# Kernel tuning notes

Hardware: AMD Instinct MI355X
Metric: run time of the kernel (lower is better)

The kernel has to match this reference:

```python
import jax, jax.numpy as jnp
import numpy as np

B, S, D = 8, 4096, 1024
F = 4 * D  # expert hidden dim (internal_dim = d_model * 4)
E = 8      # num experts


def setup_inputs() -> dict:
    key = jax.random.key(0)
    ks = jax.random.split(key, 7)
    x = jax.random.normal(ks[0], (B, S, D), dtype=jnp.float32)
    expert_weights = jax.random.uniform(ks[1], (B, 1), dtype=jnp.float32)
    expert_indices = jax.random.randint(ks[2], (B, 1), 0, E)
    # Per-expert MLP params: Linear(D,F) -> GELU -> Linear(F,D)
    W1 = jax.random.normal(ks[3], (E, D, F), dtype=jnp.float32) / np.sqrt(D)
    b1 = jnp.zeros((E, F), dtype=jnp.float32)
    W2 = jax.random.normal(ks[4], (E, F, D), dtype=jnp.float32) / np.sqrt(F)
    b2 = jnp.zeros((E, D), dtype=jnp.float32)
    return {"x": x, "expert_weights": expert_weights, "W1": W1, "b1": b1,
            "W2": W2, "b2": b2, "expert_indices": expert_indices}


def reference(x, expert_weights, W1, b1, W2, b2, expert_indices):
    # Top-1 routing per sequence (router built with top_k=1):
    # each batch element b is processed by expert idx[b], output scaled by w[b].
    idx = expert_indices[:, 0]          # [B]
    w = expert_weights[:, 0]            # [B]
    w1 = W1[idx]                        # [B, D, F] gather of expert params
    w2 = W2[idx]                        # [B, F, D]
    h = jnp.einsum('bsd,bdf->bsf', x, w1) + b1[idx][:, None, :]
    h = jax.nn.gelu(h, approximate=False)  # torch nn.GELU default = exact erf
    y = jnp.einsum('bsf,bfd->bsd', h, w2) + b2[idx][:, None, :]
    # weighted scatter-combine: final_output[mask] += expert_output * w
    return y * w[:, None, None]
```

## Files before the change

kernel.cpp:

```cpp
#include <hip/hip_runtime.h>
#include <hip/hip_bf16.h>


#define B_ 8
#define S_ 4096
#define D_ 1024
#define F_ 4096
#define E_ 8

typedef __bf16 bf16x8 __attribute__((ext_vector_type(8)));
typedef float f32x4 __attribute__((ext_vector_type(4)));

__device__ __forceinline__ unsigned short f2bf(float f) {
  unsigned u = __float_as_uint(f);
  u += 0x7FFFu + ((u >> 16) & 1u);
  return (unsigned short)(u >> 16);
}

#define GLD16(g, l) __builtin_amdgcn_global_load_lds(                         \
    (const __attribute__((address_space(1))) unsigned int*)(g),              \
    (__attribute__((address_space(3))) unsigned int*)(l), 16, 0, 0)

__global__ __launch_bounds__(256) void transpose_cvt_kernel(
    const float* __restrict__ src, unsigned short* __restrict__ dst,
    int R, int C) {
  __shared__ float t[32][33];
  const float* s = src + (size_t)blockIdx.z * R * C;
  unsigned short* d = dst + (size_t)blockIdx.z * R * C;
  int c0 = blockIdx.x * 32, r0 = blockIdx.y * 32;
  int x = threadIdx.x, y = threadIdx.y;
#pragma unroll
  for (int j = 0; j < 32; j += 8)
    t[y + j][x] = s[(size_t)(r0 + y + j) * C + (c0 + x)];
  __syncthreads();
#pragma unroll
  for (int j = 0; j < 32; j += 8)
    d[(size_t)(c0 + y + j) * R + (r0 + x)] = f2bf(t[x][y + j]);
}

__global__ __launch_bounds__(256) void cvt_bf16_kernel(
    const float* __restrict__ src, unsigned short* __restrict__ dst, long n4) {
  long i = (long)blockIdx.x * 256 + threadIdx.x;
  long stride = (long)gridDim.x * 256;
  for (; i < n4; i += stride) {
    float4 v = ((const float4*)src)[i];
    uint2 o;
    o.x = (unsigned)f2bf(v.x) | ((unsigned)f2bf(v.y) << 16);
    o.y = (unsigned)f2bf(v.z) | ((unsigned)f2bf(v.w) << 16);
    ((uint2*)dst)[i] = o;
  }
}


#define STAGE(cur, op, h, tk, base)                                           \
  {                                                                           \
    const unsigned short* g0_ = (base) + (size_t)((h) * 128 + sr) * LDK +     \
                                (tk) * 64 + sgc * 8;                          \
    GLD16(g0_, smem + (cur) * 65536 + (op) * 32768 + (h) * 16384 +            \
                   wave * 1024);                                              \
    GLD16(g0_ + (size_t)64 * LDK,                                             \
          smem + (cur) * 65536 + (op) * 32768 + (h) * 16384 + 8192 +          \
              wave * 1024);                                                   \
  }

#define LDA_HALF(cur, H)                                                      \
  _Pragma("unroll") for (int m = 0; m < 4; ++m) {                             \
    const char* p_ = smem + (cur) * 65536 + (H) * 16384 +                     \
                     (wr * 64 + m * 16 + l15) * 128;                          \
    aM[m][0] = *(const bf16x8*)(p_ + ca0);                                    \
    aM[m][1] = *(const bf16x8*)(p_ + ca1);                                    \
  }

#define LDB_Q(cur, Q, breg)                                                   \
  _Pragma("unroll") for (int n = 0; n < 2; ++n) {                             \
    const char* p_ = smem + (cur) * 65536 + 32768 + (wc >> 1) * 16384 +       \
                     ((wc & 1) * 64 + ((Q) * 2 + n) * 16 + l15) * 128;        \
    breg[n][0] = *(const bf16x8*)(p_ + ca0);                                  \
    breg[n][1] = *(const bf16x8*)(p_ + ca1);                                  \
  }

#define MMA_Q(MB, breg, NB)                                                   \
  _Pragma("unroll") for (int ks = 0; ks < 2; ++ks)                            \
      _Pragma("unroll") for (int m = 0; m < 4; ++m)                           \
          _Pragma("unroll") for (int n = 0; n < 2; ++n)                       \
              acc[(MB) + m][(NB) + n] =                                       \
      __builtin_amdgcn_mfma_f32_16x16x32_bf16(                                \
          aM[m][ks], breg[n][ks], acc[(MB) + m][(NB) + n], 0, 0, 0);

#define PH_END                                                                \
  __builtin_amdgcn_s_setprio(0);                                              \
  __builtin_amdgcn_sched_barrier(0);                                          \
  __builtin_amdgcn_s_barrier();

#define TILE(cur, t, MODE)                                                    \
  LDA_HALF(cur, 0);                                                           \
  LDB_Q(cur, 0, bq0);                                                         \
  if ((MODE) >= 1) STAGE((cur) ^ 1, 0, 1, (t) + 1, Abase);                    \
  __builtin_amdgcn_s_setprio(1);                                              \
  MMA_Q(0, bq0, 0);                                                           \
  PH_END;                                                                     \
  LDB_Q(cur, 1, bq1);                                                         \
  if ((MODE) == 2) STAGE(cur, 0, 0, (t) + 2, Abase);                          \
  __builtin_amdgcn_s_setprio(1);                                              \
  MMA_Q(0, bq1, 2);                                                           \
  PH_END;                                                                     \
  LDA_HALF(cur, 1);                                                           \
  if ((MODE) == 2) STAGE(cur, 1, 0, (t) + 2, Bbase);                          \
  __builtin_amdgcn_s_setprio(1);                                              \
  MMA_Q(4, bq0, 0);                                                           \
  PH_END;                                                                     \
  if ((MODE) == 2) STAGE(cur, 1, 1, (t) + 2, Bbase);                          \
  __builtin_amdgcn_s_setprio(1);                                              \
  MMA_Q(4, bq1, 2);                                                           \
  __builtin_amdgcn_s_setprio(0);                                              \
  __builtin_amdgcn_sched_barrier(0);                                          \
  if ((MODE) == 2) asm volatile("s_waitcnt vmcnt(6)" ::: "memory");           \
  if ((MODE) == 1) asm volatile("s_waitcnt vmcnt(0)" ::: "memory");           \
  __builtin_amdgcn_s_barrier();

template <int NT, int LDK, int NCOL, bool GELU>
__global__ __launch_bounds__(512, 2) void gemm8p_kernel(
    const unsigned short* __restrict__ A,
    const unsigned short* __restrict__ Bw,
    const float* __restrict__ bias,
    const int* __restrict__ eidx, const float* __restrict__ ew,
    void* __restrict__ Out, int grow0, int nbm) {
  extern __shared__ __align__(16) char smem[];

  const int tid = threadIdx.x;
  const int lane = tid & 63;
  const int wave = tid >> 6;
  const int wr = wave >> 2;
  const int wc = wave & 3;
  const int l15 = lane & 15, lhi = lane >> 4;

  const int nwg = nbm * (NCOL / 256);
  int wg = blockIdx.x;
  if ((nwg & 7) == 0) wg = (wg & 7) * (nwg >> 3) + (wg >> 3);
  const int bm = wg % nbm, bn = wg / nbm;

  const int bat = (grow0 + bm * 256) >> 12;
  const int e = eidx[bat];

  const unsigned short* Abase = A + (size_t)bm * 256 * LDK;
  const unsigned short* Bbase =
      Bw + (size_t)e * (F_ * D_) + (size_t)bn * 256 * LDK;

  const int sr = tid >> 3;
  const int sgc = (tid & 7) ^ (sr & 7);
  const int ca0 = ((lhi ^ (l15 & 7)) << 4);
  const int ca1 = (((4 + lhi) ^ (l15 & 7)) << 4);

  f32x4 acc[8][4] = {};
  bf16x8 aM[4][2], bq0[2][2], bq1[2][2];

  STAGE(0, 0, 0, 0, Abase);
  STAGE(0, 1, 0, 0, Bbase);
  STAGE(0, 1, 1, 0, Bbase);
  STAGE(0, 0, 1, 0, Abase);
  STAGE(1, 0, 0, 1, Abase);
  STAGE(1, 1, 0, 1, Bbase);
  STAGE(1, 1, 1, 1, Bbase);
  asm volatile("s_waitcnt vmcnt(6)" ::: "memory");
  __builtin_amdgcn_s_barrier();

#pragma unroll 1
  for (int t = 0; t < NT - 2; t += 2) {
    TILE(0, t, 2);
    TILE(1, t + 1, 2);
  }
  TILE(0, NT - 2, 1);
  TILE(1, NT - 1, 0);

  const int colbase = bn * 256 + (wc >> 1) * 128 + (wc & 1) * 64 + l15;
  float bv[4];
#pragma unroll
  for (int n = 0; n < 4; ++n) bv[n] = bias[(size_t)e * NCOL + colbase + n * 16];
  const float scale = GELU ? 1.0f : ew[bat];

#pragma unroll
  for (int m = 0; m < 8; ++m) {
    const int trow =
        (m < 4 ? wr * 64 + m * 16 : 128 + wr * 64 + (m - 4) * 16) + lhi * 4;
    const size_t rowb = (size_t)bm * 256 + trow;
#pragma unroll
    for (int r = 0; r < 4; ++r) {
      const size_t off = (rowb + r) * NCOL + colbase;
      if (GELU) {
#pragma unroll
        for (int n = 0; n < 4; ++n) {
          float v = acc[m][n][r] + bv[n];
          float zz = v * (0.79788456080286536f + 0.0356774081f * v * v);
          float g = v / (1.0f + __expf(-2.0f * zz));
          ((unsigned short*)Out)[off + n * 16] = f2bf(g);
        }
      } else {
#pragma unroll
        for (int n = 0; n < 4; ++n)
          ((float*)Out)[off + n * 16] = (acc[m][n][r] + bv[n]) * scale;
      }
    }
  }
}

extern "C" void kernel_launch(void* const* d_in, const int* in_sizes, int n_in,
                              void* d_out, int out_size, void* d_ws,
                              size_t ws_size, hipStream_t stream) {
  const float* x = (const float*)d_in[0];
  const float* ew = (const float*)d_in[1];
  const float* W1 = (const float*)d_in[2];
  const float* b1 = (const float*)d_in[3];
  const float* W2 = (const float*)d_in[4];
  const float* b2 = (const float*)d_in[5];
  const int* eidx = (const int*)d_in[6];
  float* out = (float*)d_out;

  char* ws = (char*)d_ws;
  const size_t WT = (size_t)E_ * F_ * D_ * 2;
  const size_t XB = (size_t)B_ * S_ * D_ * 2;
  unsigned short* w1t = (unsigned short*)ws;
  unsigned short* w2t = (unsigned short*)(ws + WT);

  auto g1 = gemm8p_kernel<16, D_, F_, true>;
  auto g2 = gemm8p_kernel<64, F_, D_, false>;
  hipFuncSetAttribute((const void*)g1,
                      hipFuncAttributeMaxDynamicSharedMemorySize, 131072);
  hipFuncSetAttribute((const void*)g2,
                      hipFuncAttributeMaxDynamicSharedMemorySize, 131072);

  transpose_cvt_kernel<<<dim3(F_ / 32, D_ / 32, E_), dim3(32, 8), 0, stream>>>(
      W1, w1t, D_, F_);
  transpose_cvt_kernel<<<dim3(D_ / 32, F_ / 32, E_), dim3(32, 8), 0, stream>>>(
      W2, w2t, F_, D_);

  const long total_rows = (long)B_ * S_;

  long avail = (long)ws_size - (long)(2 * WT + XB);
  long CH = avail > 0 ? (avail / ((long)F_ * 2)) : 0;
  CH = (CH / 256) * 256;
  if (CH > 16384) CH = 16384;
  if (CH > total_rows) CH = total_rows;

  if (CH >= 256) {
    unsigned short* xbf = (unsigned short*)(ws + 2 * WT);
    unsigned short* hbuf = (unsigned short*)(ws + 2 * WT + XB);
    cvt_bf16_kernel<<<2048, 256, 0, stream>>>(x, xbf, (long)B_ * S_ * D_ / 4);
    for (long r0 = 0; r0 < total_rows; r0 += CH) {
      long nr = total_rows - r0;
      if (nr > CH) nr = CH;
      int nbm = (int)(nr / 256);
      g1<<<dim3(nbm * (F_ / 256)), 512, 131072, stream>>>(
          xbf + r0 * D_, w1t, b1, eidx, ew, hbuf, (int)r0, nbm);
      g2<<<dim3(nbm * (D_ / 256)), 512, 131072, stream>>>(
          hbuf, w2t, b2, eidx, ew, out + r0 * D_, (int)r0, nbm);
    }
  } else {
    long cap = ((long)ws_size - (long)(2 * WT)) / ((long)(D_ + F_) * 2);
    long chunk = (cap / 256) * 256;
    if (chunk > total_rows) chunk = total_rows;
    if (chunk < 256) chunk = 256;
    unsigned short* xbf = (unsigned short*)(ws + 2 * WT);
    unsigned short* hbuf = xbf + (size_t)chunk * D_;
    for (long r0 = 0; r0 < total_rows; r0 += chunk) {
      long nr = total_rows - r0;
      if (nr > chunk) nr = chunk;
      cvt_bf16_kernel<<<512, 256, 0, stream>>>(x + r0 * D_, xbf, nr * D_ / 4);
      int nbm = (int)(nr / 256);
      g1<<<dim3(nbm * (F_ / 256)), 512, 131072, stream>>>(
          xbf, w1t, b1, eidx, ew, hbuf, (int)r0, nbm);
      g2<<<dim3(nbm * (D_ / 256)), 512, 131072, stream>>>(
          hbuf, w2t, b2, eidx, ew, out + r0 * D_, (int)r0, nbm);
    }
  }
}
```

Baseline: 663.2 us.

## Make GEMM1 blocks loop over four column panels with a continuous load pipeline

Each GEMM1 workgroup now computes four consecutive 256-wide output column panels. The global-to-LDS prefetch pipeline runs straight across panel boundaries, and each finished panel's accumulators are written out and zeroed inside the main loop. This removes per-block prologue and epilogue pipeline bubbles and cuts the GEMM1 grid to a quarter, at the cost of fewer workgroups and possible load imbalance or tail effects. GEMM2 keeps one panel per block.

```diff
diff --git a/kernel.cpp b/kernel.cpp
--- a/kernel.cpp
+++ b/kernel.cpp
@@ -52,15 +52,24 @@
 }
 
 
-#define STAGE(cur, op, h, tk, base)                                           \
+#define STAGE_A(cur, h, g)                                                    \
   {                                                                           \
-    const unsigned short* g0_ = (base) + (size_t)((h) * 128 + sr) * LDK +     \
-                                (tk) * 64 + sgc * 8;                          \
-    GLD16(g0_, smem + (cur) * 65536 + (op) * 32768 + (h) * 16384 +            \
-                   wave * 1024);                                              \
+    const unsigned short* g0_ = Abase + (size_t)((h) * 128 + sr) * LDK +      \
+                                ((g) & (NT - 1)) * 64 + sgc * 8;              \
+    GLD16(g0_, smem + (cur) * 65536 + (h) * 16384 + wave * 1024);             \
     GLD16(g0_ + (size_t)64 * LDK,                                             \
-          smem + (cur) * 65536 + (op) * 32768 + (h) * 16384 + 8192 +          \
-              wave * 1024);                                                   \
+          smem + (cur) * 65536 + (h) * 16384 + 8192 + wave * 1024);           \
+  }
+
+#define STAGE_B(cur, h, g)                                                    \
+  {                                                                           \
+    const unsigned short* g0_ = Bbase +                                       \
+                                (size_t)((g) >> LOGNT) * 256 * LDK +          \
+                                (size_t)((h) * 128 + sr) * LDK +              \
+                                ((g) & (NT - 1)) * 64 + sgc * 8;              \
+    GLD16(g0_, smem + (cur) * 65536 + 32768 + (h) * 16384 + wave * 1024);     \
+    GLD16(g0_ + (size_t)64 * LDK,                                             \
+          smem + (cur) * 65536 + 32768 + (h) * 16384 + 8192 + wave * 1024);   \
   }
 
 #define LDA_HALF(cur, H)                                                      \
@@ -92,24 +101,24 @@
   __builtin_amdgcn_sched_barrier(0);                                          \
   __builtin_amdgcn_s_barrier();
 
-#define TILE(cur, t, MODE)                                                    \
+#define TILE(cur, g, MODE)                                                    \
   LDA_HALF(cur, 0);                                                           \
   LDB_Q(cur, 0, bq0);                                                         \
-  if ((MODE) >= 1) STAGE((cur) ^ 1, 0, 1, (t) + 1, Abase);                    \
+  if ((MODE) >= 1) STAGE_A((cur) ^ 1, 1, (g) + 1);                            \
   __builtin_amdgcn_s_setprio(1);                                              \
   MMA_Q(0, bq0, 0);                                                           \
   PH_END;                                                                     \
   LDB_Q(cur, 1, bq1);                                                         \
-  if ((MODE) == 2) STAGE(cur, 0, 0, (t) + 2, Abase);                          \
+  if ((MODE) == 2) STAGE_A(cur, 0, (g) + 2);                                  \
   __builtin_amdgcn_s_setprio(1);                                              \
   MMA_Q(0, bq1, 2);                                                           \
   PH_END;                                                                     \
   LDA_HALF(cur, 1);                                                           \
-  if ((MODE) == 2) STAGE(cur, 1, 0, (t) + 2, Bbase);                          \
+  if ((MODE) == 2) STAGE_B(cur, 0, (g) + 2);                                  \
   __builtin_amdgcn_s_setprio(1);                                              \
   MMA_Q(4, bq0, 0);                                                           \
   PH_END;                                                                     \
-  if ((MODE) == 2) STAGE(cur, 1, 1, (t) + 2, Bbase);                          \
+  if ((MODE) == 2) STAGE_B(cur, 1, (g) + 2);                                  \
   __builtin_amdgcn_s_setprio(1);                                              \
   MMA_Q(4, bq1, 2);                                                           \
   __builtin_amdgcn_s_setprio(0);                                              \
@@ -118,7 +127,39 @@
   if ((MODE) == 1) asm volatile("s_waitcnt vmcnt(0)" ::: "memory");           \
   __builtin_amdgcn_s_barrier();
 
-template <int NT, int LDK, int NCOL, bool GELU>
+#define WRITEPANEL(p)                                                         \
+  {                                                                           \
+    const int colbase =                                                       \
+        (bn0 + (p)) * 256 + (wc >> 1) * 128 + (wc & 1) * 64 + l15;            \
+    float bv[4];                                                              \
+    _Pragma("unroll") for (int n = 0; n < 4; ++n)                             \
+        bv[n] = bias[(size_t)e * NCOL + colbase + n * 16];                    \
+    _Pragma("unroll") for (int m = 0; m < 8; ++m) {                           \
+      const int trow =                                                        \
+          (m < 4 ? wr * 64 + m * 16 : 128 + wr * 64 + (m - 4) * 16) +         \
+          lhi * 4;                                                            \
+      const size_t rowb = (size_t)bm * 256 + trow;                            \
+      _Pragma("unroll") for (int r = 0; r < 4; ++r) {                         \
+        const size_t off = (rowb + r) * NCOL + colbase;                       \
+        if (GELU) {                                                           \
+          _Pragma("unroll") for (int n = 0; n < 4; ++n) {                     \
+            float v = acc[m][n][r] + bv[n];                                   \
+            float zz = v * (0.79788456080286536f + 0.0356774081f * v * v);    \
+            float gg = v / (1.0f + __expf(-2.0f * zz));                       \
+            ((unsigned short*)Out)[off + n * 16] = f2bf(gg);                  \
+          }                                                                   \
+        } else {                                                              \
+          _Pragma("unroll") for (int n = 0; n < 4; ++n)                       \
+              ((float*)Out)[off + n * 16] = (acc[m][n][r] + bv[n]) * scale;   \
+        }                                                                     \
+      }                                                                       \
+    }                                                                         \
+    _Pragma("unroll") for (int m = 0; m < 8; ++m)                             \
+        _Pragma("unroll") for (int n = 0; n < 4; ++n)                         \
+            acc[m][n] = (f32x4){0.f, 0.f, 0.f, 0.f};                          \
+  }
+
+template <int NT, int LOGNT, int PN, int LDK, int NCOL, bool GELU>
 __global__ __launch_bounds__(512, 2) void gemm8p_kernel(
     const unsigned short* __restrict__ A,
     const unsigned short* __restrict__ Bw,
@@ -126,6 +167,7 @@
     const int* __restrict__ eidx, const float* __restrict__ ew,
     void* __restrict__ Out, int grow0, int nbm) {
   extern __shared__ __align__(16) char smem[];
+  constexpr int TOT = NT * PN;
 
   const int tid = threadIdx.x;
   const int lane = tid & 63;
@@ -134,17 +176,18 @@
   const int wc = wave & 3;
   const int l15 = lane & 15, lhi = lane >> 4;
 
-  const int nwg = nbm * (NCOL / 256);
+  const int nwg = nbm * (NCOL / 256 / PN);
   int wg = blockIdx.x;
   if ((nwg & 7) == 0) wg = (wg & 7) * (nwg >> 3) + (wg >> 3);
-  const int bm = wg % nbm, bn = wg / nbm;
+  const int bm = wg % nbm;
+  const int bn0 = (wg / nbm) * PN;
 
   const int bat = (grow0 + bm * 256) >> 12;
   const int e = eidx[bat];
 
   const unsigned short* Abase = A + (size_t)bm * 256 * LDK;
   const unsigned short* Bbase =
-      Bw + (size_t)e * (F_ * D_) + (size_t)bn * 256 * LDK;
+      Bw + (size_t)e * NCOL * LDK + (size_t)bn0 * 256 * LDK;
 
   const int sr = tid >> 3;
   const int sgc = (tid & 7) ^ (sr & 7);
@@ -153,54 +196,29 @@
 
   f32x4 acc[8][4] = {};
   bf16x8 aM[4][2], bq0[2][2], bq1[2][2];
-
-  STAGE(0, 0, 0, 0, Abase);
-  STAGE(0, 1, 0, 0, Bbase);
-  STAGE(0, 1, 1, 0, Bbase);
-  STAGE(0, 0, 1, 0, Abase);
-  STAGE(1, 0, 0, 1, Abase);
-  STAGE(1, 1, 0, 1, Bbase);
-  STAGE(1, 1, 1, 1, Bbase);
+  const float scale = GELU ? 1.0f : ew[bat];
+
+  STAGE_A(0, 0, 0);
+  STAGE_B(0, 0, 0);
+  STAGE_B(0, 1, 0);
+  STAGE_A(0, 1, 0);
+  STAGE_A(1, 0, 1);
+  STAGE_B(1, 0, 1);
+  STAGE_B(1, 1, 1);
   asm volatile("s_waitcnt vmcnt(6)" ::: "memory");
   __builtin_amdgcn_s_barrier();
 
 #pragma unroll 1
-  for (int t = 0; t < NT - 2; t += 2) {
-    TILE(0, t, 2);
-    TILE(1, t + 1, 2);
-  }
-  TILE(0, NT - 2, 1);
-  TILE(1, NT - 1, 0);
-
-  const int colbase = bn * 256 + (wc >> 1) * 128 + (wc & 1) * 64 + l15;
-  float bv[4];
-#pragma unroll
-  for (int n = 0; n < 4; ++n) bv[n] = bias[(size_t)e * NCOL + colbase + n * 16];
-  const float scale = GELU ? 1.0f : ew[bat];
-
-#pragma unroll
-  for (int m = 0; m < 8; ++m) {
-    const int trow =
-        (m < 4 ? wr * 64 + m * 16 : 128 + wr * 64 + (m - 4) * 16) + lhi * 4;
-    const size_t rowb = (size_t)bm * 256 + trow;
-#pragma unroll
-    for (int r = 0; r < 4; ++r) {
-      const size_t off = (rowb + r) * NCOL + colbase;
-      if (GELU) {
-#pragma unroll
-        for (int n = 0; n < 4; ++n) {
-          float v = acc[m][n][r] + bv[n];
-          float zz = v * (0.79788456080286536f + 0.0356774081f * v * v);
-          float g = v / (1.0f + __expf(-2.0f * zz));
-          ((unsigned short*)Out)[off + n * 16] = f2bf(g);
-        }
-      } else {
-#pragma unroll
-        for (int n = 0; n < 4; ++n)
-          ((float*)Out)[off + n * 16] = (acc[m][n][r] + bv[n]) * scale;
-      }
+  for (int g = 0; g < TOT - 2; g += 2) {
+    TILE(0, g, 2);
+    TILE(1, g + 1, 2);
+    if (PN > 1 && ((g + 1) & (NT - 1)) == (NT - 1)) {
+      WRITEPANEL((g + 1) >> LOGNT);
     }
   }
+  TILE(0, TOT - 2, 1);
+  TILE(1, TOT - 1, 0);
+  WRITEPANEL(PN - 1);
 }
 
 extern "C" void kernel_launch(void* const* d_in, const int* in_sizes, int n_in,
@@ -221,8 +239,8 @@
   unsigned short* w1t = (unsigned short*)ws;
   unsigned short* w2t = (unsigned short*)(ws + WT);
 
-  auto g1 = gemm8p_kernel<16, D_, F_, true>;
-  auto g2 = gemm8p_kernel<64, F_, D_, false>;
+  auto g1 = gemm8p_kernel<16, 4, 4, D_, F_, true>;
+  auto g2 = gemm8p_kernel<64, 6, 1, F_, D_, false>;
   hipFuncSetAttribute((const void*)g1,
                       hipFuncAttributeMaxDynamicSharedMemorySize, 131072);
   hipFuncSetAttribute((const void*)g2,
@@ -249,7 +267,7 @@
       long nr = total_rows - r0;
       if (nr > CH) nr = CH;
       int nbm = (int)(nr / 256);
-      g1<<<dim3(nbm * (F_ / 256)), 512, 131072, stream>>>(
+      g1<<<dim3(nbm * (F_ / 256 / 4)), 512, 131072, stream>>>(
           xbf + r0 * D_, w1t, b1, eidx, ew, hbuf, (int)r0, nbm);
       g2<<<dim3(nbm * (D_ / 256)), 512, 131072, stream>>>(
           hbuf, w2t, b2, eidx, ew, out + r0 * D_, (int)r0, nbm);
@@ -266,7 +284,7 @@
       if (nr > chunk) nr = chunk;
       cvt_bf16_kernel<<<512, 256, 0, stream>>>(x + r0 * D_, xbf, nr * D_ / 4);
       int nbm = (int)(nr / 256);
-      g1<<<dim3(nbm * (F_ / 256)), 512, 131072, stream>>>(
+      g1<<<dim3(nbm * (F_ / 256 / 4)), 512, 131072, stream>>>(
           xbf, w1t, b1, eidx, ew, hbuf, (int)r0, nbm);
       g2<<<dim3(nbm * (D_ / 256)), 512, 131072, stream>>>(
           hbuf, w2t, b2, eidx, ew, out + r0 * D_, (int)r0, nbm);
```

Result: slower. 689.6 us (+4.0%).
